# Kernel optimization log

Hardware: AMD Instinct MI355X
Metric: run time of the kernel (lower is better)

Reference implementation:

```python
import jax, jax.numpy as jnp
import numpy as np

B, T, DIM, DIM_EPS, H = 4, 1024, 2048, 2048, 16
HD = DIM // H        # 128, value head dim
HDE = DIM_EPS // H   # 128, q/k head dim


def setup_inputs() -> dict:
    key = jax.random.key(0)
    ks = jax.random.split(key, 6)
    s = 0.02
    # rotary frequencies as in llama-style precompute (theta=10000)
    inv_freq = 1.0 / (10000.0 ** (np.arange(0, HDE, 2, dtype=np.float32) / HDE))
    t = np.arange(T, dtype=np.float32)
    ang = np.outer(t, inv_freq)  # (T, HDE//2)
    return {
        "v": jax.random.normal(ks[0], (B, T, DIM), jnp.float32),
        "x_eps": jax.random.normal(ks[1], (B, T, DIM_EPS), jnp.float32),
        "freqs_cos": jnp.asarray(np.cos(ang)),
        "freqs_sin": jnp.asarray(np.sin(ang)),
        "W_eps_attn": jax.random.normal(ks[2], (DIM_EPS, 2 * DIM_EPS), jnp.float32) * s,
        "W_attn": jax.random.normal(ks[3], (DIM, DIM), jnp.float32) * s,
        "W_proj": jax.random.normal(ks[4], (DIM, DIM), jnp.float32) * s,
        "W_eps_proj": jax.random.normal(ks[5], (DIM_EPS, DIM_EPS), jnp.float32) * s,
    }


def _rope(x, cos, sin):
    # x: (B, T, H, HDE) -> complex-multiply by freqs_cis of shape (T, HDE//2)
    xr = x.reshape(*x.shape[:-1], -1, 2)
    x_re, x_im = xr[..., 0], xr[..., 1]
    c = cos[None, :, None, :]  # (1, T, 1, HDE//2)
    s = sin[None, :, None, :]
    o_re = x_re * c - x_im * s
    o_im = x_re * s + x_im * c
    return jnp.stack([o_re, o_im], axis=-1).reshape(x.shape)


def reference(v, x_eps, freqs_cos, freqs_sin, W_eps_attn, W_attn, W_proj, W_eps_proj):
    Bn, Tn, C = v.shape
    qk = x_eps @ W_eps_attn            # (B, T, 2*DIM_EPS)
    q, k = jnp.split(qk, 2, axis=-1)
    vp = v @ W_attn                    # (B, T, DIM)
    q = _rope(q.reshape(Bn, Tn, H, HDE), freqs_cos, freqs_sin)
    k = _rope(k.reshape(Bn, Tn, H, HDE), freqs_cos, freqs_sin)
    q = q.transpose(0, 2, 1, 3)        # (B, H, T, HDE)
    k = k.transpose(0, 2, 1, 3)
    vh = vp.reshape(Bn, Tn, H, HD).transpose(0, 2, 1, 3)
    scale = 1.0 / jnp.sqrt(jnp.asarray(HDE, q.dtype))
    scores = jnp.einsum("bhqd,bhkd->bhqk", q, k) * scale
    causal = jnp.tril(jnp.ones((Tn, Tn), bool))
    scores = jnp.where(causal[None, None], scores, jnp.finfo(scores.dtype).min)
    att = jax.nn.softmax(scores, axis=-1)
    y = jnp.einsum("bhqk,bhkd->bhqd", att, vh)
    y = y.transpose(0, 2, 1, 3).reshape(Bn, Tn, C)
    v_out = y @ W_proj
    x_eps_out = x_eps @ W_eps_proj
    return (v_out, x_eps_out)
```

## Files before the change

kernel.cpp:

```cpp
#include <hip/hip_runtime.h>
#include <stdint.h>

typedef __attribute__((ext_vector_type(8))) short  short8;
typedef __attribute__((ext_vector_type(4))) float  f32x4;
typedef __attribute__((ext_vector_type(4))) float  float4v;
typedef __attribute__((ext_vector_type(4))) unsigned short ushort4v;

#define DEV __device__ __forceinline__

DEV unsigned short f2bf(float f) {
    union { float f; unsigned int u; } x; x.f = f;
    unsigned int u = x.u;
    unsigned int r = (u + 0x7fffu + ((u >> 16) & 1u)) >> 16;
    return (unsigned short)r;
}
DEV float bf2f(unsigned short b) {
    union { unsigned int u; float f; } x; x.u = ((unsigned int)b) << 16;
    return x.f;
}

DEV void gll16(const void* g, void* l) {
    __builtin_amdgcn_global_load_lds(
        (const __attribute__((address_space(1))) void*)g,
        (__attribute__((address_space(3))) void*)l, 16, 0, 0);
}

#define MROWS 4096
#define KDIM  2048
#define NQK   4096

__global__ void cast_f32_bf16(const float* __restrict__ in,
                              unsigned short* __restrict__ out, int n4) {
    int i = blockIdx.x * blockDim.x + threadIdx.x;
    if (i < n4) {
        float4v f = ((const float4v*)in)[i];
        ushort4v o;
        o[0] = f2bf(f[0]); o[1] = f2bf(f[1]); o[2] = f2bf(f[2]); o[3] = f2bf(f[3]);
        ((ushort4v*)out)[i] = o;
    }
}

__global__ void transpose_cast(const float* __restrict__ W,
                               unsigned short* __restrict__ Wt, int K, int N) {
    __shared__ float tile[32][33];
    int tx = threadIdx.x, ty = threadIdx.y;
    int n0 = blockIdx.x * 32, k0 = blockIdx.y * 32;
#pragma unroll
    for (int j = 0; j < 32; j += 8)
        tile[ty + j][tx] = W[(size_t)(k0 + ty + j) * N + n0 + tx];
    __syncthreads();
#pragma unroll
    for (int j = 0; j < 32; j += 8)
        Wt[(size_t)(n0 + ty + j) * K + k0 + tx] = f2bf(tile[tx][ty + j]);
}

__global__ void transpose_v(const unsigned short* __restrict__ vp,
                            unsigned short* __restrict__ vpT) {
    __shared__ unsigned short tile[32][34];
    int tx = threadIdx.x, ty = threadIdx.y;
    int R0 = blockIdx.y * 32;
    int c0 = blockIdx.x * 32;
    int bh = R0 >> 7, d0 = R0 & 127;
    int b = bh >> 4, h = bh & 15;
#pragma unroll
    for (int j = 0; j < 32; j += 8)
        tile[ty + j][tx] = vp[(size_t)(b * 1024 + c0 + ty + j) * 2048 + h * 128 + d0 + tx];
    __syncthreads();
#pragma unroll
    for (int j = 0; j < 32; j += 8)
        vpT[(size_t)(R0 + ty + j) * 1024 + c0 + tx] = tile[tx][ty + j];
}

__global__ __launch_bounds__(512, 2) void gemm256(
    const unsigned short* __restrict__ A0g, const unsigned short* __restrict__ B0g,
    float* __restrict__ Cf0, unsigned short* __restrict__ Ch0,
    int N0, int tx0, int nb0, int outbf0,
    const unsigned short* __restrict__ A1g, const unsigned short* __restrict__ B1g,
    float* __restrict__ Cf1, unsigned short* __restrict__ Ch1,
    int N1, int tx1, int outbf1, int K) {

    __shared__ __align__(16) char lds[131072];

    int blk = blockIdx.x;
    const unsigned short* Ag; const unsigned short* Bg;
    float* Cf; unsigned short* Ch; int N, tx, outbf, nwg;
    if (blk < nb0) { Ag = A0g; Bg = B0g; Cf = Cf0; Ch = Ch0; N = N0; tx = tx0; outbf = outbf0; nwg = nb0; }
    else { blk -= nb0; Ag = A1g; Bg = B1g; Cf = Cf1; Ch = Ch1; N = N1; tx = tx1; outbf = outbf1; nwg = gridDim.x - nb0; }
    { int cpx = nwg >> 3; blk = (blk & 7) * cpx + (blk >> 3); }
    const int bx = blk % tx, by = blk / tx;

    const int tid = threadIdx.x;
    const int lane = tid & 63;
    const int w  = tid >> 6;
    const int lr = lane & 15, lk = lane >> 4;
    const int wm = w >> 2, wn = w & 3;
    const int cswz16 = (lk ^ ((lr >> 3) << 1)) * 16;
    const int rdOff  = lr * 64 + cswz16;
    const int bRow0B = (wn & 1) * 4096;

    const unsigned short* Arow = Ag + (size_t)(by * 256) * K;
    const unsigned short* Brow = Bg + (size_t)(bx * 256) * K;

    const int srow = tid >> 2;
    const int sclog = (tid & 3) ^ (((tid >> 5) & 1) << 1);
    const unsigned short* aSt0 = Arow + (size_t)srow * K + sclog * 8;
    const unsigned short* aSt1 = aSt0 + (size_t)128 * K;
    const unsigned short* bSt0 = Brow + (size_t)srow * K + sclog * 8;
    const unsigned short* bSt1 = bSt0 + (size_t)128 * K;

    char* sA0 = lds;            char* sB0 = lds + 32768;
    char* sA1 = lds + 65536;    char* sB1 = lds + 98304;
    const int sOff = tid * 16;

    const char* aB0 = lds + wm * 16384;
    const char* aB1 = aB0 + 65536;
    const char* bB0 = lds + 32768 + (wn >> 1) * 16384;
    const char* bB1 = bB0 + 65536;

    f32x4 acc[8][4];
#pragma unroll
    for (int m = 0; m < 8; ++m)
#pragma unroll
        for (int n = 0; n < 4; ++n) acc[m][n] = (f32x4){0.f, 0.f, 0.f, 0.f};

    const int NT = K >> 6;

    gll16(bSt0,      sB0 + sOff);                 gll16(bSt0 + 32, sB0 + 8192 + sOff);
    gll16(bSt1,      sB0 + 16384 + sOff);         gll16(bSt1 + 32, sB0 + 16384 + 8192 + sOff);
    gll16(aSt0,      sA0 + sOff);                 gll16(aSt0 + 32, sA0 + 8192 + sOff);
    gll16(aSt1,      sA0 + 16384 + sOff);         gll16(aSt1 + 32, sA0 + 16384 + 8192 + sOff);
    gll16(bSt0 + 64, sB1 + sOff);                 gll16(bSt0 + 96, sB1 + 8192 + sOff);
    asm volatile("s_waitcnt vmcnt(2)" ::: "memory");
    __builtin_amdgcn_s_barrier();

#define MFMA_BF(a, b, c) __builtin_amdgcn_mfma_f32_16x16x32_bf16(a, b, c, 0, 0, 0)

#define LD4A(DST, BASE, KS, MH)                                                  \
    DST[0] = *(const short8*)((BASE) + (KS) * 8192 + (MH) * 4096 +    0 + rdOff); \
    DST[1] = *(const short8*)((BASE) + (KS) * 8192 + (MH) * 4096 + 1024 + rdOff); \
    DST[2] = *(const short8*)((BASE) + (KS) * 8192 + (MH) * 4096 + 2048 + rdOff); \
    DST[3] = *(const short8*)((BASE) + (KS) * 8192 + (MH) * 4096 + 3072 + rdOff);

#define LD4B(DST, BASE, KS)                                                               \
    DST[0] = *(const short8*)((BASE) + (KS) * 8192 + bRow0B +    0 + rdOff);              \
    DST[1] = *(const short8*)((BASE) + (KS) * 8192 + bRow0B + 1024 + rdOff);              \
    DST[2] = *(const short8*)((BASE) + (KS) * 8192 + bRow0B + 2048 + rdOff);              \
    DST[3] = *(const short8*)((BASE) + (KS) * 8192 + bRow0B + 3072 + rdOff);

#define MFMA16(MH, AR, BR)                                                  \
    __builtin_amdgcn_s_setprio(1);                                          \
    _Pragma("unroll")                                                       \
    for (int i = 0; i < 4; ++i)                                             \
        _Pragma("unroll")                                                   \
        for (int nf = 0; nf < 4; ++nf)                                      \
            acc[(MH) * 4 + i][nf] = MFMA_BF(AR[i], BR[nf], acc[(MH) * 4 + i][nf]); \
    __builtin_amdgcn_s_setprio(0);

#define PHASE_SYNC                                          \
    asm volatile("s_waitcnt lgkmcnt(8)" ::: "memory");      \
    __builtin_amdgcn_s_barrier();                           \
    __builtin_amdgcn_sched_barrier(0);

    short8 Ax[4], Ay[4], Bx[4], By[4];
    LD4A(Ax, aB0, 0, 0)
    LD4B(Bx, bB0, 0)

    for (int u = 0; u < NT; ++u) {
        const bool par = u & 1;
        const char* aC = par ? aB1 : aB0;
        const char* bC = par ? bB1 : bB0;
        const char* aN = par ? aB0 : aB1;
        const char* bN = par ? bB0 : bB1;
        char* dAN = par ? sA0 : sA1;
        char* dBN = par ? sB0 : sB1;
        char* dBC = par ? sB1 : sB0;
        const int kA  = (u + 1 < NT ? u + 1 : NT - 1) * 64;
        const int kB2 = (u + 2 < NT ? u + 2 : NT - 1) * 64;

        LD4A(Ay, aC, 1, 0)
        LD4B(By, bC, 1)
        gll16(bSt1 + kA,      dBN + 16384 + sOff);
        gll16(bSt1 + kA + 32, dBN + 16384 + 8192 + sOff);
        gll16(aSt0 + kA,      dAN + sOff);
        gll16(aSt0 + kA + 32, dAN + 8192 + sOff);
        gll16(aSt1 + kA,      dAN + 16384 + sOff);
        gll16(aSt1 + kA + 32, dAN + 16384 + 8192 + sOff);
        PHASE_SYNC
        MFMA16(0, Ax, Bx)
        __builtin_amdgcn_s_barrier();

        LD4A(Ax, aC, 0, 1)
        LD4B(Bx, bC, 0)
        PHASE_SYNC
        MFMA16(0, Ay, By)
        __builtin_amdgcn_s_barrier();

        LD4A(Ay, aC, 1, 1)
        LD4B(By, bC, 1)
        PHASE_SYNC
        MFMA16(1, Ax, Bx)
        asm volatile("s_waitcnt vmcnt(0)" ::: "memory");
        __builtin_amdgcn_s_barrier();

        LD4A(Ax, aN, 0, 0)
        LD4B(Bx, bN, 0)
        gll16(bSt0 + kB2,      dBC + sOff);
        gll16(bSt0 + kB2 + 32, dBC + 8192 + sOff);
        PHASE_SYNC
        MFMA16(1, Ay, By)
        __builtin_amdgcn_s_barrier();
    }
    asm volatile("s_waitcnt vmcnt(0)" ::: "memory");
#undef LD4A
#undef LD4B
#undef MFMA16
#undef PHASE_SYNC

    if (outbf) {
#pragma unroll
        for (int mf = 0; mf < 8; ++mf)
#pragma unroll
            for (int nf = 0; nf < 4; ++nf)
#pragma unroll
                for (int r = 0; r < 4; ++r) {
                    int row = by * 256 + wm * 128 + mf * 16 + lk * 4 + r;
                    int col = bx * 256 + wn * 64 + nf * 16 + lr;
                    Ch[(size_t)row * N + col] = f2bf(acc[mf][nf][r]);
                }
    } else {
#pragma unroll
        for (int mf = 0; mf < 8; ++mf)
#pragma unroll
            for (int nf = 0; nf < 4; ++nf)
#pragma unroll
                for (int r = 0; r < 4; ++r) {
                    int row = by * 256 + wm * 128 + mf * 16 + lk * 4 + r;
                    int col = bx * 256 + wn * 64 + nf * 16 + lr;
                    Cf[(size_t)row * N + col] = acc[mf][nf][r];
                }
    }
}

__global__ void rope_kernel(unsigned short* __restrict__ qk,
                            const float* __restrict__ fcos,
                            const float* __restrict__ fsin) {
    int idx  = blockIdx.x * 256 + threadIdx.x;
    int row  = idx >> 9;
    int g    = idx & 511;
    int t    = row & 1023;
    int half = g >> 8;
    int hp   = g & 255;
    int h    = hp >> 4;
    int ig   = hp & 15;
    int col  = half * 2048 + h * 128 + ig * 8;
    size_t off = (size_t)row * 4096 + col;

    short8 v = *(short8*)(qk + off);
    int i0 = ig * 4;
    float4v c = *(const float4v*)(fcos + t * 64 + i0);
    float4v s = *(const float4v*)(fsin + t * 64 + i0);
    short8 o;
#pragma unroll
    for (int p = 0; p < 4; ++p) {
        float re = bf2f((unsigned short)v[2 * p]);
        float im = bf2f((unsigned short)v[2 * p + 1]);
        o[2 * p]     = (short)f2bf(re * c[p] - im * s[p]);
        o[2 * p + 1] = (short)f2bf(re * s[p] + im * c[p]);
    }
    *(short8*)(qk + off) = o;
}

__global__ __launch_bounds__(256) void attn_kernel(
    const unsigned short* __restrict__ qk,
    const unsigned short* __restrict__ vpT,
    unsigned short* __restrict__ y) {

    const int bh = blockIdx.x;
    const int qt = 7 - (int)blockIdx.y;
    const int b = bh >> 4, h = bh & 15;
    const int qb0 = qt * 128;

    __shared__ __align__(16) unsigned short Kt[64 * 128];
    __shared__ __align__(16) unsigned short Vt[128 * 64];
    __shared__ __align__(16) unsigned short Pl[4 * 32 * 72];

    const int tid = threadIdx.x, w = tid >> 6, lane = tid & 63;
    const int lr = lane & 15, lk = lane >> 4;

    const unsigned short* Qb = qk + (size_t)(b * 1024) * 4096 + h * 128;
    const unsigned short* Kb = Qb + 2048;
    const unsigned short* Vg = vpT + (size_t)bh * 128 * 1024;
    unsigned short* Pw = &Pl[w * 32 * 72];

    short8 qf[2][4];
#pragma unroll
    for (int m = 0; m < 2; ++m) {
        const unsigned short* qrow = Qb + (size_t)(qb0 + w * 32 + m * 16 + lr) * 4096;
#pragma unroll
        for (int db = 0; db < 4; ++db)
            qf[m][db] = *(const short8*)(qrow + db * 32 + lk * 8);
    }

    f32x4 acc[2][8];
#pragma unroll
    for (int m = 0; m < 2; ++m)
#pragma unroll
        for (int n = 0; n < 8; ++n) acc[m][n] = (f32x4){0.f, 0.f, 0.f, 0.f};
    float m_i[2][4], l_i[2][4];
#pragma unroll
    for (int m = 0; m < 2; ++m)
#pragma unroll
        for (int r = 0; r < 4; ++r) { m_i[m][r] = -1e30f; l_i[m][r] = 0.f; }

    const int nkt = 2 * qt + 2;
    for (int kt = 0; kt < nkt; ++kt) {
#pragma unroll
        for (int c = 0; c < 4; ++c) {
            int base = w * 4096 + c * 1024;
            int row  = (base >> 8) + (lane >> 4);
            int colB = (lane & 15) * 16;
            int scol = colB ^ ((row & 7) << 4);
            gll16(Kb + (size_t)(kt * 64 + row) * 4096 + (scol >> 1),
                  (char*)Kt + base);
        }
#pragma unroll
        for (int c = 0; c < 4; ++c) {
            int base = w * 4096 + c * 1024;
            int d    = (base >> 7) + (lane >> 3);
            int colB = (lane & 7) * 16;
            int scol = colB ^ ((d & 7) << 4);
            gll16(Vg + (size_t)d * 1024 + kt * 64 + (scol >> 1),
                  (char*)Vt + base);
        }
        __syncthreads();

        f32x4 s[2][4];
#pragma unroll
        for (int m = 0; m < 2; ++m)
#pragma unroll
            for (int n = 0; n < 4; ++n) s[m][n] = (f32x4){0.f, 0.f, 0.f, 0.f};
#pragma unroll
        for (int db = 0; db < 4; ++db)
#pragma unroll
            for (int n = 0; n < 4; ++n) {
                int krow = n * 16 + lr;
                int cb = (db * 64 + lk * 16) ^ ((krow & 7) << 4);
                short8 kf = *(const short8*)((const char*)Kt + krow * 256 + cb);
                s[0][n] = __builtin_amdgcn_mfma_f32_16x16x32_bf16(qf[0][db], kf, s[0][n], 0, 0, 0);
                s[1][n] = __builtin_amdgcn_mfma_f32_16x16x32_bf16(qf[1][db], kf, s[1][n], 0, 0, 0);
            }

        const float sc = 0.08838834764831845f;
        const bool diag = (kt >= 2 * qt);
#pragma unroll
        for (int m = 0; m < 2; ++m)
#pragma unroll
            for (int n = 0; n < 4; ++n)
#pragma unroll
                for (int r = 0; r < 4; ++r) {
                    float v = s[m][n][r] * sc;
                    if (diag) {
                        int q   = qb0 + w * 32 + m * 16 + lk * 4 + r;
                        int key = kt * 64 + n * 16 + lr;
                        if (key > q) v = -1e30f;
                    }
                    s[m][n][r] = v;
                }

#pragma unroll
        for (int m = 0; m < 2; ++m) {
            float pm[4];
#pragma unroll
            for (int r = 0; r < 4; ++r)
                pm[r] = fmaxf(fmaxf(s[m][0][r], s[m][1][r]), fmaxf(s[m][2][r], s[m][3][r]));
#pragma unroll
            for (int o = 1; o < 16; o <<= 1)
#pragma unroll
                for (int r = 0; r < 4; ++r)
                    pm[r] = fmaxf(pm[r], __shfl_xor(pm[r], o, 16));

            float resc[4], rs[4];
#pragma unroll
            for (int r = 0; r < 4; ++r) {
                float mn = fmaxf(m_i[m][r], pm[r]);
                resc[r] = __expf(m_i[m][r] - mn);
                m_i[m][r] = mn;
                rs[r] = 0.f;
            }
#pragma unroll
            for (int n = 0; n < 4; ++n)
#pragma unroll
                for (int r = 0; r < 4; ++r) {
                    float p = __expf(s[m][n][r] - m_i[m][r]);
                    s[m][n][r] = p;
                    rs[r] += p;
                }
#pragma unroll
            for (int o = 1; o < 16; o <<= 1)
#pragma unroll
                for (int r = 0; r < 4; ++r)
                    rs[r] += __shfl_xor(rs[r], o, 16);
#pragma unroll
            for (int r = 0; r < 4; ++r)
                l_i[m][r] = l_i[m][r] * resc[r] + rs[r];
#pragma unroll
            for (int n = 0; n < 8; ++n)
#pragma unroll
                for (int r = 0; r < 4; ++r)
                    acc[m][n][r] *= resc[r];

#pragma unroll
            for (int n = 0; n < 4; ++n)
#pragma unroll
                for (int r = 0; r < 4; ++r)
                    Pw[(m * 16 + lk * 4 + r) * 72 + n * 16 + lr] = f2bf(s[m][n][r]);
        }

#pragma unroll
        for (int ks = 0; ks < 2; ++ks) {
            short8 pf0 = *(const short8*)&Pw[(lr) * 72 + ks * 32 + lk * 8];
            short8 pf1 = *(const short8*)&Pw[(16 + lr) * 72 + ks * 32 + lk * 8];
#pragma unroll
            for (int n8 = 0; n8 < 8; ++n8) {
                int d  = n8 * 16 + lr;
                int cb = (ks * 64 + lk * 16) ^ ((d & 7) << 4);
                short8 vf = *(const short8*)((const char*)Vt + d * 128 + cb);
                acc[0][n8] = __builtin_amdgcn_mfma_f32_16x16x32_bf16(pf0, vf, acc[0][n8], 0, 0, 0);
                acc[1][n8] = __builtin_amdgcn_mfma_f32_16x16x32_bf16(pf1, vf, acc[1][n8], 0, 0, 0);
            }
        }
        __syncthreads();
    }

    unsigned short* yb = y + (size_t)(b * 1024) * 2048 + h * 128;
#pragma unroll
    for (int m = 0; m < 2; ++m)
#pragma unroll
        for (int n8 = 0; n8 < 8; ++n8)
#pragma unroll
            for (int r = 0; r < 4; ++r) {
                int t = qb0 + w * 32 + m * 16 + lk * 4 + r;
                int d = n8 * 16 + lr;
                yb[(size_t)t * 2048 + d] = f2bf(acc[m][n8][r] / l_i[m][r]);
            }
}

extern "C" void kernel_launch(void* const* d_in, const int* in_sizes, int n_in,
                              void* d_out, int out_size, void* d_ws, size_t ws_size,
                              hipStream_t stream) {
    const float* v_in  = (const float*)d_in[0];
    const float* xeps  = (const float*)d_in[1];
    const float* fcos  = (const float*)d_in[2];
    const float* fsin  = (const float*)d_in[3];
    const float* Wea   = (const float*)d_in[4];
    const float* Wa    = (const float*)d_in[5];
    const float* Wp    = (const float*)d_in[6];
    const float* Wep   = (const float*)d_in[7];
    float* out = (float*)d_out;

    char* ws = (char*)d_ws;
    unsigned short* xe16 = (unsigned short*)ws;  ws += (size_t)MROWS * KDIM * 2;
    unsigned short* v16  = (unsigned short*)ws;  ws += (size_t)MROWS * KDIM * 2;
    unsigned short* WeaT = (unsigned short*)ws;  ws += (size_t)NQK * KDIM * 2;
    unsigned short* WaT  = (unsigned short*)ws;  ws += (size_t)KDIM * KDIM * 2;
    unsigned short* WpT  = (unsigned short*)ws;  ws += (size_t)KDIM * KDIM * 2;
    unsigned short* WepT = (unsigned short*)ws;  ws += (size_t)KDIM * KDIM * 2;
    unsigned short* qk16 = (unsigned short*)ws;  ws += (size_t)MROWS * NQK * 2;
    unsigned short* vp16 = (unsigned short*)ws;  ws += (size_t)MROWS * KDIM * 2;
    unsigned short* y16  = (unsigned short*)ws;  ws += (size_t)MROWS * KDIM * 2;
    unsigned short* vpT  = v16;

    cast_f32_bf16<<<8192, 256, 0, stream>>>(xeps, xe16, MROWS * KDIM / 4);
    cast_f32_bf16<<<8192, 256, 0, stream>>>(v_in, v16,  MROWS * KDIM / 4);

    transpose_cast<<<dim3(NQK / 32, KDIM / 32), dim3(32, 8), 0, stream>>>(Wea, WeaT, KDIM, NQK);
    transpose_cast<<<dim3(KDIM / 32, KDIM / 32), dim3(32, 8), 0, stream>>>(Wa,  WaT,  KDIM, KDIM);
    transpose_cast<<<dim3(KDIM / 32, KDIM / 32), dim3(32, 8), 0, stream>>>(Wp,  WpT,  KDIM, KDIM);
    transpose_cast<<<dim3(KDIM / 32, KDIM / 32), dim3(32, 8), 0, stream>>>(Wep, WepT, KDIM, KDIM);

    gemm256<<<256, 512, 0, stream>>>(
        xe16, WeaT, nullptr, qk16, NQK, 16, 256, 1,
        xe16, WeaT, nullptr, qk16, NQK, 16, 1, KDIM);

    rope_kernel<<<8192, 256, 0, stream>>>(qk16, fcos, fsin);

    gemm256<<<256, 512, 0, stream>>>(
        v16,  WaT,  nullptr, vp16, KDIM, 8, 128, 1,
        xe16, WepT, out + (size_t)MROWS * KDIM, nullptr, KDIM, 8, 0, KDIM);

    transpose_v<<<dim3(1024 / 32, 8192 / 32), dim3(32, 8), 0, stream>>>(vp16, vpT);

    attn_kernel<<<dim3(64, 8), 256, 0, stream>>>(qk16, vpT, y16);

    gemm256<<<128, 512, 0, stream>>>(
        y16, WpT, out, nullptr, KDIM, 8, 128, 0,
        y16, WpT, out, nullptr, KDIM, 8, 0, KDIM);
}
```

Before: 338.2 us.

## Restructure GEMM main loop into eight-phase quadrant schedule with reordered staging

Rewrites the bf16 GEMM inner loop so each K-tile pair runs as eight phases. Each phase computes one 4x2 fragment quadrant over both K-halves, reads only the LDS fragments it needs, and issues part of the next tiles' global-to-LDS staging. The prefetch order changes to stage A ahead of B, and the waits become full lgkmcnt(0) waits plus vmcnt(2) at half-tile boundaries. The aim is a more even spread of LDS reads, global loads and MFMA work across barriers, at the cost of more barriers per tile. The loop also assumes NT is even.

```diff
diff --git a/kernel.cpp b/kernel.cpp
--- a/kernel.cpp
+++ b/kernel.cpp
@@ -125,96 +125,85 @@
 
     const int NT = K >> 6;
 
-    gll16(bSt0,      sB0 + sOff);                 gll16(bSt0 + 32, sB0 + 8192 + sOff);
-    gll16(bSt1,      sB0 + 16384 + sOff);         gll16(bSt1 + 32, sB0 + 16384 + 8192 + sOff);
-    gll16(aSt0,      sA0 + sOff);                 gll16(aSt0 + 32, sA0 + 8192 + sOff);
-    gll16(aSt1,      sA0 + 16384 + sOff);         gll16(aSt1 + 32, sA0 + 16384 + 8192 + sOff);
-    gll16(bSt0 + 64, sB1 + sOff);                 gll16(bSt0 + 96, sB1 + 8192 + sOff);
+    auto STAGE = [&](const unsigned short* srcHalf, int k0, char* ldsHalf) {
+        gll16(srcHalf + k0,      ldsHalf + sOff);
+        gll16(srcHalf + k0 + 32, ldsHalf + 8192 + sOff);
+    };
+
+    STAGE(aSt0, 0, sA0);  STAGE(aSt1, 0, sA0 + 16384);
+    STAGE(bSt0, 0, sB0);  STAGE(bSt1, 0, sB0 + 16384);
+    STAGE(aSt0, 64, sA1);
     asm volatile("s_waitcnt vmcnt(2)" ::: "memory");
     __builtin_amdgcn_s_barrier();
 
 #define MFMA_BF(a, b, c) __builtin_amdgcn_mfma_f32_16x16x32_bf16(a, b, c, 0, 0, 0)
 
-#define LD4A(DST, BASE, KS, MH)                                                  \
-    DST[0] = *(const short8*)((BASE) + (KS) * 8192 + (MH) * 4096 +    0 + rdOff); \
-    DST[1] = *(const short8*)((BASE) + (KS) * 8192 + (MH) * 4096 + 1024 + rdOff); \
-    DST[2] = *(const short8*)((BASE) + (KS) * 8192 + (MH) * 4096 + 2048 + rdOff); \
-    DST[3] = *(const short8*)((BASE) + (KS) * 8192 + (MH) * 4096 + 3072 + rdOff);
-
-#define LD4B(DST, BASE, KS)                                                               \
-    DST[0] = *(const short8*)((BASE) + (KS) * 8192 + bRow0B +    0 + rdOff);              \
-    DST[1] = *(const short8*)((BASE) + (KS) * 8192 + bRow0B + 1024 + rdOff);              \
-    DST[2] = *(const short8*)((BASE) + (KS) * 8192 + bRow0B + 2048 + rdOff);              \
-    DST[3] = *(const short8*)((BASE) + (KS) * 8192 + bRow0B + 3072 + rdOff);
-
-#define MFMA16(MH, AR, BR)                                                  \
-    __builtin_amdgcn_s_setprio(1);                                          \
-    _Pragma("unroll")                                                       \
-    for (int i = 0; i < 4; ++i)                                             \
-        _Pragma("unroll")                                                   \
-        for (int nf = 0; nf < 4; ++nf)                                      \
-            acc[(MH) * 4 + i][nf] = MFMA_BF(AR[i], BR[nf], acc[(MH) * 4 + i][nf]); \
+#define RD_A(BASE, MH)                                                              \
+    _Pragma("unroll") for (int i = 0; i < 4; ++i) {                                 \
+        Ar[i][0] = *(const short8*)((BASE) +        (MH) * 4096 + i * 1024 + rdOff); \
+        Ar[i][1] = *(const short8*)((BASE) + 8192 + (MH) * 4096 + i * 1024 + rdOff); \
+    }
+
+#define RD_B(BASE, NH)                                                                        \
+    _Pragma("unroll") for (int j = 0; j < 2; ++j) {                                           \
+        Br[j][0] = *(const short8*)((BASE) +        bRow0B + ((NH) * 2 + j) * 1024 + rdOff);  \
+        Br[j][1] = *(const short8*)((BASE) + 8192 + bRow0B + ((NH) * 2 + j) * 1024 + rdOff);  \
+    }
+
+#define MFMA16(MH, NH)                                                       \
+    __builtin_amdgcn_s_setprio(1);                                           \
+    _Pragma("unroll") for (int ks = 0; ks < 2; ++ks)                         \
+        _Pragma("unroll") for (int i = 0; i < 4; ++i)                        \
+            _Pragma("unroll") for (int j = 0; j < 2; ++j)                    \
+                acc[(MH) * 4 + i][(NH) * 2 + j] =                            \
+                    MFMA_BF(Ar[i][ks], Br[j][ks], acc[(MH) * 4 + i][(NH) * 2 + j]); \
     __builtin_amdgcn_s_setprio(0);
 
-#define PHASE_SYNC                                          \
-    asm volatile("s_waitcnt lgkmcnt(8)" ::: "memory");      \
-    __builtin_amdgcn_s_barrier();                           \
-    __builtin_amdgcn_sched_barrier(0);
-
-    short8 Ax[4], Ay[4], Bx[4], By[4];
-    LD4A(Ax, aB0, 0, 0)
-    LD4B(Bx, bB0, 0)
-
-    for (int u = 0; u < NT; ++u) {
-        const bool par = u & 1;
-        const char* aC = par ? aB1 : aB0;
-        const char* bC = par ? bB1 : bB0;
-        const char* aN = par ? aB0 : aB1;
-        const char* bN = par ? bB0 : bB1;
-        char* dAN = par ? sA0 : sA1;
-        char* dBN = par ? sB0 : sB1;
-        char* dBC = par ? sB1 : sB0;
-        const int kA  = (u + 1 < NT ? u + 1 : NT - 1) * 64;
-        const int kB2 = (u + 2 < NT ? u + 2 : NT - 1) * 64;
-
-        LD4A(Ay, aC, 1, 0)
-        LD4B(By, bC, 1)
-        gll16(bSt1 + kA,      dBN + 16384 + sOff);
-        gll16(bSt1 + kA + 32, dBN + 16384 + 8192 + sOff);
-        gll16(aSt0 + kA,      dAN + sOff);
-        gll16(aSt0 + kA + 32, dAN + 8192 + sOff);
-        gll16(aSt1 + kA,      dAN + 16384 + sOff);
-        gll16(aSt1 + kA + 32, dAN + 16384 + 8192 + sOff);
-        PHASE_SYNC
-        MFMA16(0, Ax, Bx)
-        __builtin_amdgcn_s_barrier();
-
-        LD4A(Ax, aC, 0, 1)
-        LD4B(Bx, bC, 0)
-        PHASE_SYNC
-        MFMA16(0, Ay, By)
-        __builtin_amdgcn_s_barrier();
-
-        LD4A(Ay, aC, 1, 1)
-        LD4B(By, bC, 1)
-        PHASE_SYNC
-        MFMA16(1, Ax, Bx)
-        asm volatile("s_waitcnt vmcnt(0)" ::: "memory");
-        __builtin_amdgcn_s_barrier();
-
-        LD4A(Ax, aN, 0, 0)
-        LD4B(Bx, bN, 0)
-        gll16(bSt0 + kB2,      dBC + sOff);
-        gll16(bSt0 + kB2 + 32, dBC + 8192 + sOff);
-        PHASE_SYNC
-        MFMA16(1, Ay, By)
-        __builtin_amdgcn_s_barrier();
+#define PH(RDS, STG, MFMAQ, VMW)                               \
+    {                                                          \
+        RDS;                                                   \
+        STG;                                                   \
+        __builtin_amdgcn_s_barrier();                          \
+        asm volatile("s_waitcnt lgkmcnt(0)" ::: "memory");     \
+        __builtin_amdgcn_sched_barrier(0);                     \
+        MFMAQ;                                                 \
+        VMW;                                                   \
+        __builtin_amdgcn_s_barrier();                          \
+    }
+
+#define VMC2 asm volatile("s_waitcnt vmcnt(2)" ::: "memory")
+
+    short8 Ar[4][2], Br[2][2];
+
+    for (int i2 = 0; i2 < NT; i2 += 2) {
+        const int kt1 = (i2 + 1) * 64;
+        const int kA  = (i2 + 2 < NT ? i2 + 2 : NT - 1) * 64;
+        const int kA3 = (i2 + 3 < NT ? i2 + 3 : NT - 1) * 64;
+
+        PH({ RD_A(aB0, 0) RD_B(bB0, 0) },
+           { STAGE(aSt1, kt1, sA1 + 16384); STAGE(bSt0, kt1, sB1); STAGE(bSt1, kt1, sB1 + 16384); },
+           MFMA16(0, 0), {})
+        PH({ RD_B(bB0, 1) }, {}, MFMA16(0, 1), {})
+        PH({ RD_A(aB0, 1) RD_B(bB0, 0) }, {}, MFMA16(1, 0), {})
+        PH({ RD_B(bB0, 1) },
+           { STAGE(aSt0, kA, sA0); },
+           MFMA16(1, 1), VMC2)
+
+        PH({ RD_A(aB1, 0) RD_B(bB1, 0) },
+           { STAGE(aSt1, kA, sA0 + 16384); STAGE(bSt0, kA, sB0); STAGE(bSt1, kA, sB0 + 16384); },
+           MFMA16(0, 0), {})
+        PH({ RD_B(bB1, 1) }, {}, MFMA16(0, 1), {})
+        PH({ RD_A(aB1, 1) RD_B(bB1, 0) }, {}, MFMA16(1, 0), {})
+        PH({ RD_B(bB1, 1) },
+           { STAGE(aSt0, kA3, sA1); },
+           MFMA16(1, 1), VMC2)
     }
     asm volatile("s_waitcnt vmcnt(0)" ::: "memory");
-#undef LD4A
-#undef LD4B
+#undef RD_A
+#undef RD_B
 #undef MFMA16
-#undef PHASE_SYNC
+#undef PH
+#undef VMC2
 
     if (outbf) {
 #pragma unroll
```

After: 329.4 us. 1.03x faster.
